# Kernel tuning notes

Hardware: AMD Instinct MI355X
Metric: run time of the kernel (lower is better)

## Reference

```python
import jax, jax.numpy as jnp
import numpy as np

B, S, D, H, BLK = 2, 4096, 1024, 16, 64

def setup_inputs() -> dict:
    key = jax.random.key(0)
    ks = jax.random.split(key, 6)
    sc = 0.02
    nb = S // BLK
    g_tok = 128
    ng = g_tok // BLK
    n_mid = nb - ng - 2
    return {
        "tokens": jax.random.normal(ks[0], (B, S, D), dtype=jnp.float32),
        "band_mask": jnp.ones((B, 1, n_mid, BLK, 3 * BLK), dtype=jnp.float32),
        "from_mask": jnp.ones((B, 1, S, 1), dtype=jnp.float32),
        "to_mask": jnp.ones((B, 1, 1, S), dtype=jnp.float32),
        "Wq": jax.random.normal(ks[1], (D, D), dtype=jnp.float32) * sc,
        "Wk": jax.random.normal(ks[2], (D, D), dtype=jnp.float32) * sc,
        "Wv": jax.random.normal(ks[3], (D, D), dtype=jnp.float32) * sc,
        "Wu": jax.random.normal(ks[4], (D, D), dtype=jnp.float32) * sc,
        "bu": jnp.zeros((D,), dtype=jnp.float32),
        "num_global_tokens": 128,
    }

def _forward(tokens, band_mask, from_mask, to_mask, Wq, Wk, Wv, Wu, bu, g):
    b, s, dm = tokens.shape
    h, blk = H, BLK
    d = dm // h
    nb = s // blk
    ng = g // blk
    rs = 1.0 / (d ** 0.5)
    pen = -10000.0

    def heads(x):
        return x.reshape(b, s, h, d).transpose(0, 2, 1, 3)  # (b,h,s,d)

    q = heads(tokens @ Wq)
    k = heads(tokens @ Wk)
    v = heads(tokens @ Wv)
    bq = q.reshape(b, h, nb, blk, d)
    bk = k.reshape(b, h, nb, blk, d)
    bv = v.reshape(b, h, nb, blk, d)

    # --- global (first) block rows: attend to everything ---
    fp = jnp.einsum('bhqd,bhkd->bhqk', q[:, :, :g], k) * rs + (1.0 - to_mask) * pen
    fw = jax.nn.softmax(fp, axis=-1)
    first = jnp.einsum('bhqk,bhkd->bhqd', fw, v).reshape(b, h, ng, blk, d)

    # --- second block: global keys + first 3 non-global blocks ---
    q1 = min(3, nb - ng)
    st = ng * blk
    k2 = jnp.concatenate([k[:, :, :g], k[:, :, st:st + q1 * blk]], axis=2)
    v2 = jnp.concatenate([v[:, :, :g], v[:, :, st:st + q1 * blk]], axis=2)
    p2 = jnp.einsum('bhqd,bhkd->bhqk', bq[:, :, ng], k2) * rs
    p2 = p2 + (1.0 - to_mask[:, :, :, :blk * (ng + q1)]) * pen
    c2 = jnp.einsum('bhqk,bhkd->bhqd', jax.nn.softmax(p2, axis=-1), v2)[:, :, None]

    # --- middle blocks: sliding window (prev, self, next) + global keys ---
    m = nb - ng - 2
    ek = jnp.concatenate([bk[:, :, ng:ng + m], bk[:, :, ng + 1:ng + 1 + m],
                          bk[:, :, ng + 2:ng + 2 + m]], axis=3)  # (b,h,m,3*blk,d)
    ev = jnp.concatenate([bv[:, :, ng:ng + m], bv[:, :, ng + 1:ng + 1 + m],
                          bv[:, :, ng + 2:ng + 2 + m]], axis=3)
    mq = bq[:, :, ng + 1:ng + 1 + m]  # (b,h,m,blk,d)
    inner = jnp.einsum('bhmqd,bhmkd->bhmqk', mq, ek) * rs + (1.0 - band_mask) * pen
    fb = jnp.einsum('bhmqd,bhkd->bhmqk', mq, k[:, :, :g]) * rs
    fb = fb + (1.0 - to_mask[:, :, :, :g][:, :, :, None, :]) * pen
    aw = jax.nn.softmax(jnp.concatenate([fb, inner], axis=-1), axis=-1)
    cm = (jnp.einsum('bhmqk,bhmkd->bhmqd', aw[..., g:], ev)
          + jnp.einsum('bhmqk,bhkd->bhmqd', aw[..., :g], v[:, :, :g]))

    # --- last block: global keys + last 3 blocks ---
    ql = min(3, nb - ng)
    kl = jnp.concatenate([k[:, :, :g], k[:, :, -(ql * blk):]], axis=2)
    vl = jnp.concatenate([v[:, :, :g], v[:, :, -(ql * blk):]], axis=2)
    lm = jnp.concatenate([to_mask[:, :, :, :g], to_mask[:, :, :, -(ql * blk):]], axis=3)
    pl = jnp.einsum('bhqd,bhkd->bhqk', bq[:, :, -1], kl) * rs + (1.0 - lm) * pen
    cl = jnp.einsum('bhqk,bhkd->bhqd', jax.nn.softmax(pl, axis=-1), vl)[:, :, None]

    ctx = jnp.concatenate([first, c2, cm, cl], axis=2).reshape(b, h, s, d) * from_mask
    ctx = ctx.transpose(0, 2, 1, 3).reshape(b, s, dm)
    return ctx @ Wu + bu

def reference(tokens, band_mask, from_mask, to_mask, Wq, Wk, Wv, Wu, bu, num_global_tokens):
    return _forward(tokens, band_mask, from_mask, to_mask, Wq, Wk, Wv, Wu, bu, num_global_tokens)
```

## Files before the change

### kernel.cpp

```cpp
#include <hip/hip_runtime.h>

typedef unsigned short u16;
using bfrag = __attribute__((ext_vector_type(8))) short;
using f32x4 = __attribute__((ext_vector_type(4))) float;

#define PEN  (-10000.0f)
#define RSC  (0.125f)

__device__ __forceinline__ u16 f2bf(float f) {
  union { float f; unsigned u; } v; v.f = f;
  unsigned r = v.u + 0x7fffu + ((v.u >> 16) & 1u);
  return (u16)(r >> 16);
}

__device__ __forceinline__ void gload16(const u16* g, u16* l) {
  __builtin_amdgcn_global_load_lds(
      (const __attribute__((address_space(1))) unsigned int*)g,
      (__attribute__((address_space(3))) unsigned int*)l, 16, 0, 0);
}

__global__ __launch_bounds__(256) void prep_k(
    const float* __restrict__ tokens, u16* __restrict__ tok_bf,
    const float* __restrict__ w0, const float* __restrict__ w1,
    const float* __restrict__ w2, const float* __restrict__ w3,
    u16* __restrict__ wt) {
  __shared__ float tile[64][65];
  int id = blockIdx.x, t = threadIdx.x;
  if (id < 8192) {
    int i = id * 256 + t;
    float4 v = ((const float4*)tokens)[i];
    u16 o[4] = { f2bf(v.x), f2bf(v.y), f2bf(v.z), f2bf(v.w) };
    *(uint2*)(tok_bf + (size_t)i * 4) = *(uint2*)o;
    return;
  }
  int wid = id - 8192;
  int z = wid >> 8, rem = wid & 255;
  const float* W = (z == 0) ? w0 : (z == 1) ? w1 : (z == 2) ? w2 : w3;
  u16* out = wt + (size_t)z * 1024 * 1024;
  int k0 = (rem & 15) * 64, n0 = (rem >> 4) * 64;
#pragma unroll
  for (int i = 0; i < 16; ++i) {
    int idx = i * 256 + t, kk = idx >> 6, nn = idx & 63;
    tile[nn][kk] = W[(size_t)(k0 + kk) * 1024 + n0 + nn];
  }
  __syncthreads();
#pragma unroll
  for (int i = 0; i < 16; ++i) {
    int idx = i * 256 + t, nn = idx >> 6, kk = idx & 63;
    out[(size_t)(n0 + nn) * 1024 + k0 + kk] = f2bf(tile[nn][kk]);
  }
}

__global__ __launch_bounds__(256) void gemm_qkv_k(
    const u16* __restrict__ A, const u16* __restrict__ WT,
    u16* __restrict__ Q, u16* __restrict__ K, u16* __restrict__ VT) {
  __shared__ alignas(16) u16 smem[17408];
  u16* As = smem;
  u16* Bs = smem + 8192;
  int t = threadIdx.x;
  int n0 = blockIdx.x * 128, r0 = blockIdx.y * 128;
  int wave = t >> 6, lane = t & 63, quad = lane >> 4, lcol = lane & 15;
  int wr = wave & 1, wc = wave >> 1;
  int rsel = lane >> 3;
  int sseg = (lane & 7) ^ rsel;
  f32x4 acc[4][4];
#pragma unroll
  for (int mt = 0; mt < 4; ++mt)
#pragma unroll
    for (int nt = 0; nt < 4; ++nt) acc[mt][nt] = (f32x4){0.f, 0.f, 0.f, 0.f};

  const u16* a0 = A + (size_t)r0 * 1024 + sseg * 8;
  const u16* b0 = WT + (size_t)n0 * 1024 + sseg * 8;
  int sw = lcol & 7;

  for (int kt = 0; kt < 16; ++kt) {
#pragma unroll
    for (int i = 0; i < 4; ++i) {
      int ii = wave * 4 + i;
      int row = ii * 8 + rsel;
      gload16(a0 + (size_t)row * 1024 + kt * 64, As + ii * 512);
      gload16(b0 + (size_t)row * 1024 + kt * 64, Bs + ii * 512);
    }
    __syncthreads();
#pragma unroll
    for (int kh = 0; kh < 2; ++kh) {
      int seg = ((kh * 4 + quad) ^ sw) * 8;
      bfrag af[4], bf[4];
#pragma unroll
      for (int x = 0; x < 4; ++x) {
        af[x] = *(const bfrag*)(As + (wr * 64 + x * 16 + lcol) * 64 + seg);
        bf[x] = *(const bfrag*)(Bs + (wc * 64 + x * 16 + lcol) * 64 + seg);
      }
#pragma unroll
      for (int mt = 0; mt < 4; ++mt)
#pragma unroll
        for (int nt = 0; nt < 4; ++nt)
          acc[mt][nt] = __builtin_amdgcn_mfma_f32_16x16x32_bf16(af[mt], bf[nt], acc[mt][nt], 0, 0, 0);
    }
    __syncthreads();
  }
  u16 (*Cs)[136] = (u16(*)[136])smem;
#pragma unroll
  for (int mt = 0; mt < 4; ++mt)
#pragma unroll
    for (int nt = 0; nt < 4; ++nt)
#pragma unroll
      for (int r = 0; r < 4; ++r)
        Cs[wr * 64 + mt * 16 + quad * 4 + r][wc * 64 + nt * 16 + lcol] = f2bf(acc[mt][nt][r]);
  __syncthreads();
  int which = n0 >> 10;
  int b = r0 >> 12, s0v = r0 & 4095;
  if (which < 2) {
    int row = t >> 1, seg = t & 1;
    int h = ((n0 & 1023) >> 6) + seg;
    u16* outp = (which == 0 ? Q : K) + (((size_t)(b * 16 + h) * 4096 + s0v + row) << 6);
#pragma unroll
    for (int jj = 0; jj < 8; ++jj)
      *(uint4*)(outp + jj * 8) = *(uint4*)&Cs[row][seg * 64 + jj * 8];
  } else {
    int c = t & 127, h = ((n0 & 1023) >> 6) + (c >> 6), d = c & 63;
    u16* vtrow = VT + ((size_t)(b * 16 + h) << 18) + ((size_t)d << 12) + s0v;
    int sgb = t >> 7;
#pragma unroll
    for (int i = 0; i < 8; ++i) {
      int sg = sgb + 2 * i;
      u16 tmp[8];
#pragma unroll
      for (int rr = 0; rr < 8; ++rr) tmp[rr] = Cs[sg * 8 + rr][c];
      *(uint4*)(vtrow + sg * 8) = *(uint4*)tmp;
    }
  }
}

__global__ __launch_bounds__(256) void attn_k(
    const u16* __restrict__ Qg, const u16* __restrict__ Kg, const u16* __restrict__ VTg,
    const float* __restrict__ band_mask, const float* __restrict__ from_mask,
    const float* __restrict__ to_mask, u16* __restrict__ ctx,
    float* __restrict__ Opart, float* __restrict__ lbuf) {
  __shared__ alignas(16) u16 QPs[4096];
  __shared__ alignas(16) u16 Ks[2][4096];
  __shared__ alignas(16) u16 VTs[2][4096];

  int t = threadIdx.x;
  int wave = t >> 6, lane = t & 63, quad = lane >> 4, lcol = lane & 15;
  int rsel = lane >> 3, sseg = (lane & 7) ^ rsel;
  int sw = lcol & 7;
  int bh = blockIdx.y, b = bh >> 4;
  bool is_band = blockIdx.x < 62;
  int j, chunk = 0, nit, sb = 0;
  if (is_band) {
    j = blockIdx.x + 2; nit = 5;
    sb = (j == 2) ? 2 : ((j == 63) ? 61 : j - 1);
  } else {
    int jc = blockIdx.x - 62; j = jc >> 3; chunk = jc & 7; nit = 8;
  }
  bool bandmask_blk = is_band && (j >= 3) && (j <= 62);

  const u16* kbase = Kg + (((size_t)bh * 4096) << 6) + sseg * 8;
  const u16* vbase = VTg + ((size_t)bh << 18) + sseg * 8;

  auto kb_of = [&](int it) {
    return is_band ? ((it < 2) ? it : (sb + it - 2)) : (chunk * 8 + it);
  };
  auto stage = [&](int kb, int buf) {
#pragma unroll
    for (int i = 0; i < 2; ++i) {
      int ii = wave * 2 + i;
      int row = ii * 8 + rsel;
      gload16(kbase + (((size_t)kb * 64 + row) << 6), &Ks[buf][ii * 512]);
      gload16(vbase + ((size_t)row << 12) + kb * 64, &VTs[buf][ii * 512]);
    }
  };

  {
    const u16* qsrc = Qg + (((size_t)bh * 4096 + j * 64) << 6) + sseg * 8;
#pragma unroll
    for (int i = 0; i < 2; ++i) {
      int ii = wave * 2 + i;
      gload16(qsrc + (ii * 8 + rsel) * 64, &QPs[ii * 512]);
    }
  }
  stage(kb_of(0), 0);
  __syncthreads();

  bfrag qf[2];
#pragma unroll
  for (int kh = 0; kh < 2; ++kh)
    qf[kh] = *(const bfrag*)&QPs[(wave * 16 + lcol) * 64 + ((kh * 4 + quad) ^ sw) * 8];
  __syncthreads();

  float l_part[4] = {0.f, 0.f, 0.f, 0.f};
  f32x4 oa[4];
#pragma unroll
  for (int nt = 0; nt < 4; ++nt) oa[nt] = (f32x4){0.f, 0.f, 0.f, 0.f};

  int poff = lcol & 7;
  int hb = lcol >> 3;
  int q1_4 = (quad & 1) * 4;

  for (int it = 0; it < nit; ++it) {
    int buf = it & 1;
    if (it + 1 < nit) stage(kb_of(it + 1), buf ^ 1);
    int kb = kb_of(it);

    f32x4 sc[4];
#pragma unroll
    for (int nt = 0; nt < 4; ++nt) sc[nt] = (f32x4){0.f, 0.f, 0.f, 0.f};
#pragma unroll
    for (int kh = 0; kh < 2; ++kh) {
      int seg = ((kh * 4 + quad) ^ sw) * 8;
#pragma unroll
      for (int nt = 0; nt < 4; ++nt) {
        bfrag kf = *(const bfrag*)&Ks[buf][(nt * 16 + lcol) * 64 + seg];
        sc[nt] = __builtin_amdgcn_mfma_f32_16x16x32_bf16(qf[kh], kf, sc[nt], 0, 0, 0);
      }
    }

    bool use_band = bandmask_blk && (it >= 2);
    if (!use_band) {
#pragma unroll
      for (int nt = 0; nt < 4; ++nt) {
        float tm = to_mask[b * 4096 + kb * 64 + nt * 16 + lcol];
        float pn = (1.0f - tm) * PEN;
#pragma unroll
        for (int r = 0; r < 4; ++r) {
          float p = __expf(sc[nt][r] * RSC + pn);
          l_part[r] += p;
          int pseg = (nt * 2 + hb) ^ (q1_4 + r);
          QPs[(wave * 16 + quad * 4 + r) * 64 + pseg * 8 + poff] = f2bf(p);
        }
      }
    } else {
      const float* bm = band_mask + (((size_t)b * 60 + (j - 3)) << 6) * 192 + (it - 2) * 64;
#pragma unroll
      for (int r = 0; r < 4; ++r) {
        int qrow = wave * 16 + quad * 4 + r;
#pragma unroll
        for (int nt = 0; nt < 4; ++nt) {
          float msk = bm[(size_t)qrow * 192 + nt * 16 + lcol];
          float p = __expf(sc[nt][r] * RSC + (1.0f - msk) * PEN);
          l_part[r] += p;
          int pseg = (nt * 2 + hb) ^ (q1_4 + r);
          QPs[qrow * 64 + pseg * 8 + poff] = f2bf(p);
        }
      }
    }
    __syncthreads();

#pragma unroll
    for (int kh = 0; kh < 2; ++kh) {
      int seg = ((kh * 4 + quad) ^ sw) * 8;
      bfrag pf = *(const bfrag*)&QPs[(wave * 16 + lcol) * 64 + seg];
#pragma unroll
      for (int nt = 0; nt < 4; ++nt) {
        bfrag vf = *(const bfrag*)&VTs[buf][(nt * 16 + lcol) * 64 + seg];
        oa[nt] = __builtin_amdgcn_mfma_f32_16x16x32_bf16(pf, vf, oa[nt], 0, 0, 0);
      }
    }
    __syncthreads();
  }

  if (is_band) {
    float sc_r[4];
#pragma unroll
    for (int r = 0; r < 4; ++r) {
#pragma unroll
      for (int d = 1; d < 16; d <<= 1) l_part[r] += __shfl_xor(l_part[r], d);
      int qrow = wave * 16 + quad * 4 + r;
      sc_r[r] = from_mask[b * 4096 + j * 64 + qrow] / l_part[r];
    }
#pragma unroll
    for (int nt = 0; nt < 4; ++nt)
#pragma unroll
      for (int r = 0; r < 4; ++r) {
        int pseg = (nt * 2 + hb) ^ (q1_4 + r);
        QPs[(wave * 16 + quad * 4 + r) * 64 + pseg * 8 + poff] = f2bf(oa[nt][r] * sc_r[r]);
      }
    __syncthreads();
    u16* dst = ctx + (((size_t)bh * 4096 + j * 64) << 6);
#pragma unroll
    for (int i = 0; i < 2; ++i) {
      int idx = i * 256 + t, row = idx >> 3, s = idx & 7;
      *(uint4*)(dst + row * 64 + s * 8) = *(uint4*)&QPs[row * 64 + (s ^ (row & 7)) * 8];
    }
  } else {
    size_t base = (((size_t)(bh * 2 + j) * 8 + chunk) << 6);
#pragma unroll
    for (int nt = 0; nt < 4; ++nt)
#pragma unroll
      for (int r = 0; r < 4; ++r) {
        int row = wave * 16 + quad * 4 + r;
        Opart[((base + row) << 6) + nt * 16 + lcol] = oa[nt][r];
      }
#pragma unroll
    for (int r = 0; r < 4; ++r) {
#pragma unroll
      for (int d = 1; d < 16; d <<= 1) l_part[r] += __shfl_xor(l_part[r], d);
    }
    if (lcol == 0) {
#pragma unroll
      for (int r = 0; r < 4; ++r)
        lbuf[base + wave * 16 + quad * 4 + r] = l_part[r];
    }
  }
}

__global__ __launch_bounds__(256) void attn_combine_k(
    const float* __restrict__ Opart, const float* __restrict__ lbuf,
    const float* __restrict__ from_mask, u16* __restrict__ ctx) {
  int blk = blockIdx.x;
  int bh = blk >> 1, j = blk & 1, b = bh >> 4;
  int t = threadIdx.x;
  int row = t >> 2, dseg = (t & 3) << 4;

  float lt = 0.0f;
  float acc[16];
#pragma unroll
  for (int u = 0; u < 16; ++u) acc[u] = 0.0f;
#pragma unroll
  for (int c = 0; c < 8; ++c) {
    size_t rbase = (((size_t)blk * 8 + c) << 6) + row;
    lt += lbuf[rbase];
    const float* op = Opart + (rbase << 6) + dseg;
#pragma unroll
    for (int u = 0; u < 4; ++u) {
      float4 v = *(const float4*)(op + u * 4);
      acc[u * 4 + 0] += v.x;
      acc[u * 4 + 1] += v.y;
      acc[u * 4 + 2] += v.z;
      acc[u * 4 + 3] += v.w;
    }
  }
  float inv = from_mask[b * 4096 + j * 64 + row] / lt;
  u16* dst = ctx + (((size_t)bh * 4096 + j * 64 + row) << 6) + dseg;
  u16 o[8];
#pragma unroll
  for (int u = 0; u < 8; ++u) o[u] = f2bf(acc[u] * inv);
  *(uint4*)dst = *(uint4*)o;
#pragma unroll
  for (int u = 0; u < 8; ++u) o[u] = f2bf(acc[8 + u] * inv);
  *(uint4*)(dst + 8) = *(uint4*)o;
}

__global__ __launch_bounds__(256) void gemm_out_k(
    const u16* __restrict__ ctx, const u16* __restrict__ WTu,
    const float* __restrict__ bu, float* __restrict__ out) {
  __shared__ alignas(16) u16 smem[16384];
  u16* As = smem;
  u16* Bs = smem + 8192;
  int t = threadIdx.x;
  int n0 = blockIdx.x * 128, r0 = blockIdx.y * 128;
  int wave = t >> 6, lane = t & 63, quad = lane >> 4, lcol = lane & 15;
  int wr = wave & 1, wc = wave >> 1;
  int b = r0 >> 12, s0 = r0 & 4095;
  int rsel = lane >> 3;
  int sseg = (lane & 7) ^ rsel;
  int sw = lcol & 7;
  f32x4 acc[4][4];
#pragma unroll
  for (int mt = 0; mt < 4; ++mt)
#pragma unroll
    for (int nt = 0; nt < 4; ++nt) acc[mt][nt] = (f32x4){0.f, 0.f, 0.f, 0.f};

  const u16* b0 = WTu + (size_t)n0 * 1024 + sseg * 8;
  for (int kt = 0; kt < 16; ++kt) {
    const u16* a0 = ctx + (((size_t)(b * 16 + kt) * 4096 + s0) << 6) + sseg * 8;
#pragma unroll
    for (int i = 0; i < 4; ++i) {
      int ii = wave * 4 + i;
      int row = ii * 8 + rsel;
      gload16(a0 + (size_t)row * 64, As + ii * 512);
      gload16(b0 + (size_t)row * 1024 + kt * 64, Bs + ii * 512);
    }
    __syncthreads();
#pragma unroll
    for (int kh = 0; kh < 2; ++kh) {
      int seg = ((kh * 4 + quad) ^ sw) * 8;
      bfrag af[4], bf[4];
#pragma unroll
      for (int x = 0; x < 4; ++x) {
        af[x] = *(const bfrag*)(As + (wr * 64 + x * 16 + lcol) * 64 + seg);
        bf[x] = *(const bfrag*)(Bs + (wc * 64 + x * 16 + lcol) * 64 + seg);
      }
#pragma unroll
      for (int mt = 0; mt < 4; ++mt)
#pragma unroll
        for (int nt = 0; nt < 4; ++nt)
          acc[mt][nt] = __builtin_amdgcn_mfma_f32_16x16x32_bf16(af[mt], bf[nt], acc[mt][nt], 0, 0, 0);
    }
    __syncthreads();
  }
#pragma unroll
  for (int nt = 0; nt < 4; ++nt) {
    int n = n0 + wc * 64 + nt * 16 + lcol;
    float bv = bu[n];
#pragma unroll
    for (int mt = 0; mt < 4; ++mt)
#pragma unroll
      for (int r = 0; r < 4; ++r)
        out[(size_t)(r0 + wr * 64 + mt * 16 + quad * 4 + r) * 1024 + n] = acc[mt][nt][r] + bv;
  }
}

extern "C" void kernel_launch(void* const* d_in, const int* in_sizes, int n_in,
                              void* d_out, int out_size, void* d_ws, size_t ws_size,
                              hipStream_t stream) {
  const float* tokens    = (const float*)d_in[0];
  const float* band_mask = (const float*)d_in[1];
  const float* from_mask = (const float*)d_in[2];
  const float* to_mask   = (const float*)d_in[3];
  const float* Wq = (const float*)d_in[4];
  const float* Wk = (const float*)d_in[5];
  const float* Wv = (const float*)d_in[6];
  const float* Wu = (const float*)d_in[7];
  const float* bu = (const float*)d_in[8];
  float* out = (float*)d_out;

  char* ws = (char*)d_ws;
  u16* tok_bf = (u16*)(ws);
  u16* WT     = (u16*)(ws + 16777216);
  u16* Qb     = (u16*)(ws + 16777216 + 8388608);
  u16* Kb     = Qb + 8388608;
  u16* VTb    = Kb + 8388608;
  u16* ctx    = VTb + 8388608;
  float* Opart = (float*)(ctx + 8388608);
  float* lb    = Opart + (size_t)32 * 2 * 8 * 64 * 64;

  prep_k<<<9216, 256, 0, stream>>>(tokens, tok_bf, Wq, Wk, Wv, Wu, WT);
  gemm_qkv_k<<<dim3(24, 64), 256, 0, stream>>>(tok_bf, WT, Qb, Kb, VTb);
  attn_k<<<dim3(78, 32), 256, 0, stream>>>(Qb, Kb, VTb, band_mask, from_mask, to_mask,
                                           ctx, Opart, lb);
  attn_combine_k<<<64, 256, 0, stream>>>(Opart, lb, from_mask, ctx);
  gemm_out_k<<<dim3(8, 64), 256, 0, stream>>>(ctx, WT + (size_t)3 * 1024 * 1024, bu, out);
}
```

Baseline: 268.9 us.

## Stage K/V tiles through registers and use one barrier per iteration

Replaces the direct global-to-LDS async loads with ordinary vector loads into registers. Each next tile is prefetched into registers one iteration ahead and written to the double-buffered LDS at the start of the following iteration. The loop now has one __syncthreads instead of two, since P rows are written and read only by the owning wave, and the separate Q-fragment barrier is folded into the first iteration. This aims to cut barrier stalls and overlap global latency with compute, at the cost of extra VGPRs and explicit LDS store instructions.

```diff
diff --git a/kernel.cpp b/kernel.cpp
--- a/kernel.cpp
+++ b/kernel.cpp
@@ -143,7 +143,6 @@
 
   int t = threadIdx.x;
   int wave = t >> 6, lane = t & 63, quad = lane >> 4, lcol = lane & 15;
-  int rsel = lane >> 3, sseg = (lane & 7) ^ rsel;
   int sw = lcol & 7;
   int bh = blockIdx.y, b = bh >> 4;
   bool is_band = blockIdx.x < 62;
@@ -156,43 +155,42 @@
   }
   bool bandmask_blk = is_band && (j >= 3) && (j <= 62);
 
+  int srow0 = t >> 3, srow1 = 32 + srow0, sseg = t & 7;
+  int lds0 = srow0 * 64 + ((sseg ^ (srow0 & 7)) << 3);
+  int lds1 = srow1 * 64 + ((sseg ^ (srow1 & 7)) << 3);
   const u16* kbase = Kg + (((size_t)bh * 4096) << 6) + sseg * 8;
   const u16* vbase = VTg + ((size_t)bh << 18) + sseg * 8;
 
   auto kb_of = [&](int it) {
     return is_band ? ((it < 2) ? it : (sb + it - 2)) : (chunk * 8 + it);
   };
-  auto stage = [&](int kb, int buf) {
-#pragma unroll
-    for (int i = 0; i < 2; ++i) {
-      int ii = wave * 2 + i;
-      int row = ii * 8 + rsel;
-      gload16(kbase + (((size_t)kb * 64 + row) << 6), &Ks[buf][ii * 512]);
-      gload16(vbase + ((size_t)row << 12) + kb * 64, &VTs[buf][ii * 512]);
-    }
+
+  uint4 kr0, kr1, vr0, vr1;
+  auto load_tile = [&](int kb) {
+    kr0 = *(const uint4*)(kbase + (((size_t)kb * 64 + srow0) << 6));
+    kr1 = *(const uint4*)(kbase + (((size_t)kb * 64 + srow1) << 6));
+    vr0 = *(const uint4*)(vbase + ((size_t)srow0 << 12) + kb * 64);
+    vr1 = *(const uint4*)(vbase + ((size_t)srow1 << 12) + kb * 64);
+  };
+  auto write_tile = [&](int buf) {
+    *(uint4*)&Ks[buf][lds0] = kr0;  *(uint4*)&Ks[buf][lds1] = kr1;
+    *(uint4*)&VTs[buf][lds0] = vr0; *(uint4*)&VTs[buf][lds1] = vr1;
   };
 
   {
     const u16* qsrc = Qg + (((size_t)bh * 4096 + j * 64) << 6) + sseg * 8;
-#pragma unroll
-    for (int i = 0; i < 2; ++i) {
-      int ii = wave * 2 + i;
-      gload16(qsrc + (ii * 8 + rsel) * 64, &QPs[ii * 512]);
-    }
-  }
-  stage(kb_of(0), 0);
-  __syncthreads();
-
-  bfrag qf[2];
-#pragma unroll
-  for (int kh = 0; kh < 2; ++kh)
-    qf[kh] = *(const bfrag*)&QPs[(wave * 16 + lcol) * 64 + ((kh * 4 + quad) ^ sw) * 8];
-  __syncthreads();
+    uint4 q0 = *(const uint4*)(qsrc + srow0 * 64);
+    uint4 q1 = *(const uint4*)(qsrc + srow1 * 64);
+    *(uint4*)&QPs[lds0] = q0; *(uint4*)&QPs[lds1] = q1;
+    load_tile(kb_of(0));
+    write_tile(0);
+  }
 
   float l_part[4] = {0.f, 0.f, 0.f, 0.f};
   f32x4 oa[4];
 #pragma unroll
   for (int nt = 0; nt < 4; ++nt) oa[nt] = (f32x4){0.f, 0.f, 0.f, 0.f};
+  bfrag qf[2];
 
   int poff = lcol & 7;
   int hb = lcol >> 3;
@@ -200,7 +198,14 @@
 
   for (int it = 0; it < nit; ++it) {
     int buf = it & 1;
-    if (it + 1 < nit) stage(kb_of(it + 1), buf ^ 1);
+    if (it > 0) write_tile(buf);
+    if (it + 1 < nit) load_tile(kb_of(it + 1));
+    __syncthreads();
+    if (it == 0) {
+#pragma unroll
+      for (int kh = 0; kh < 2; ++kh)
+        qf[kh] = *(const bfrag*)&QPs[(wave * 16 + lcol) * 64 + (((kh * 4 + quad) ^ sw) << 3)];
+    }
     int kb = kb_of(it);
 
     f32x4 sc[4];
@@ -208,7 +213,7 @@
     for (int nt = 0; nt < 4; ++nt) sc[nt] = (f32x4){0.f, 0.f, 0.f, 0.f};
 #pragma unroll
     for (int kh = 0; kh < 2; ++kh) {
-      int seg = ((kh * 4 + quad) ^ sw) * 8;
+      int seg = ((kh * 4 + quad) ^ sw) << 3;
 #pragma unroll
       for (int nt = 0; nt < 4; ++nt) {
         bfrag kf = *(const bfrag*)&Ks[buf][(nt * 16 + lcol) * 64 + seg];
@@ -245,11 +250,10 @@
         }
       }
     }
-    __syncthreads();
 
 #pragma unroll
     for (int kh = 0; kh < 2; ++kh) {
-      int seg = ((kh * 4 + quad) ^ sw) * 8;
+      int seg = ((kh * 4 + quad) ^ sw) << 3;
       bfrag pf = *(const bfrag*)&QPs[(wave * 16 + lcol) * 64 + seg];
 #pragma unroll
       for (int nt = 0; nt < 4; ++nt) {
@@ -257,7 +261,6 @@
         oa[nt] = __builtin_amdgcn_mfma_f32_16x16x32_bf16(pf, vf, oa[nt], 0, 0, 0);
       }
     }
-    __syncthreads();
   }
 
   if (is_band) {
@@ -281,7 +284,7 @@
 #pragma unroll
     for (int i = 0; i < 2; ++i) {
       int idx = i * 256 + t, row = idx >> 3, s = idx & 7;
-      *(uint4*)(dst + row * 64 + s * 8) = *(uint4*)&QPs[row * 64 + (s ^ (row & 7)) * 8];
+      *(uint4*)(dst + row * 64 + s * 8) = *(uint4*)&QPs[row * 64 + ((s ^ (row & 7)) << 3)];
     }
   } else {
     size_t base = (((size_t)(bh * 2 + j) * 8 + chunk) << 6);
```

Result: faster. 263.4 us (-2.1%).
